# Optimization experiments

Hardware: AMD Instinct MI355X
Metric: run time of the kernel (lower is better)

The kernel has to match this reference:

```python
import jax, jax.numpy as jnp
import numpy as np

N = 8192          # num_nodes
F_IN = 512        # num_features
D = 256           # embedding_dim
C = 40            # num_classes
E = 262144        # num_edges (avg degree 32)
ALPHA = 0.5
LN_EPS = 1e-5


def _layer_norm(x, eps=LN_EPS):
    # F.layer_norm over last dim, no affine params
    mu = jnp.mean(x, axis=-1, keepdims=True)
    var = jnp.var(x, axis=-1, keepdims=True)
    return (x - mu) * jax.lax.rsqrt(var + eps)


def setup_inputs() -> dict:
    key = jax.random.key(0)
    ks = jax.random.split(key, 16)
    s_in = 1.0 / np.sqrt(F_IN)
    s_d = 1.0 / np.sqrt(D)
    inp = {
        "X": jax.random.normal(ks[0], (N, F_IN), dtype=jnp.float32),
        "edge_row": jnp.sort(jax.random.randint(ks[1], (E,), 0, N)),
        "edge_col": jax.random.randint(ks[2], (E,), 0, N),
        "edge_weight": jax.random.uniform(ks[3], (E,), dtype=jnp.float32),
        # MLP embedding: Linear(F_IN, D)
        "W_emb": jax.random.uniform(ks[4], (F_IN, D), minval=-s_in, maxval=s_in),
        "b_emb": jax.random.uniform(ks[5], (D,), minval=-s_in, maxval=s_in),
        # attention projections: Linear(D, D) x3
        "W_q": jax.random.uniform(ks[6], (D, D), minval=-s_d, maxval=s_d),
        "b_q": jax.random.uniform(ks[7], (D,), minval=-s_d, maxval=s_d),
        "W_k": jax.random.uniform(ks[8], (D, D), minval=-s_d, maxval=s_d),
        "b_k": jax.random.uniform(ks[9], (D,), minval=-s_d, maxval=s_d),
        "W_v": jax.random.uniform(ks[10], (D, D), minval=-s_d, maxval=s_d),
        "b_v": jax.random.uniform(ks[11], (D,), minval=-s_d, maxval=s_d),
        # GNN linear: Linear(D, D)
        "W_gnn": jax.random.uniform(ks[12], (D, D), minval=-s_d, maxval=s_d),
        "b_gnn": jax.random.uniform(ks[13], (D,), minval=-s_d, maxval=s_d),
        # classifier: Linear(D, C)
        "W_cls": jax.random.uniform(ks[14], (D, C), minval=-s_d, maxval=s_d),
        "b_cls": jax.random.uniform(ks[15], (C,), minval=-s_d, maxval=s_d),
    }
    return inp


def reference(X, edge_row, edge_col, edge_weight,
              W_emb, b_emb, W_q, b_q, W_k, b_k, W_v, b_v,
              W_gnn, b_gnn, W_cls, b_cls):
    # embedding MLP
    Z0 = X @ W_emb + b_emb                      # [N, D]
    # global attention with QK layer-norm
    Q = _layer_norm(Z0 @ W_q + b_q)             # [N, D]
    K = _layer_norm(Z0 @ W_k + b_k)             # [N, D]
    V = Z0 @ W_v + b_v                          # [N, D]
    scores = Q @ K.T                            # [N, N]
    attn = jax.nn.softmax(scores, axis=-1)      # [N, N]
    Z_A = attn @ V                              # [N, D]
    # sparse GNN branch: spmm(A, linear(Z0))
    H = Z0 @ W_gnn + b_gnn                      # [N, D]
    msg = H[edge_col] * edge_weight[:, None]    # [E, D]
    gnn_out = jax.ops.segment_sum(msg, edge_row, num_segments=N)  # [N, D]
    # weighted blend + classifier
    Z_out = (1.0 - ALPHA) * Z_A + ALPHA * gnn_out
    Y_hat = Z_out @ W_cls + b_cls               # [N, C]
    return (Y_hat, attn)
```

## Files before the change

### kernel.cpp

```cpp
#include <hip/hip_runtime.h>
#include <hip/hip_bf16.h>

#define N_NODES 8192
#define F_IN    512
#define DIM     256
#define NCLS    40

typedef __attribute__((ext_vector_type(8))) short bf16x8;
typedef __attribute__((ext_vector_type(4))) float f32x4;

#define MFMA16 __builtin_amdgcn_mfma_f32_16x16x32_bf16

static __device__ __forceinline__ unsigned short f2bf(float x) {
    __hip_bfloat16 h = __float2bfloat16(x);
    return *reinterpret_cast<unsigned short*>(&h);
}
static __device__ __forceinline__ float bf2f(unsigned short u) {
    union { unsigned int u32; float f; } v; v.u32 = ((unsigned int)u) << 16;
    return v.f;
}
static __device__ __forceinline__ void gll16(const void* g, void* l) {
    __builtin_amdgcn_global_load_lds(
        (const __attribute__((address_space(1))) unsigned int*)g,
        (__attribute__((address_space(3))) unsigned int*)l, 16, 0, 0);
}

__global__ __launch_bounds__(256) void split_kernel(
    const float* __restrict__ X,
    unsigned short* __restrict__ Xh, unsigned short* __restrict__ Xl)
{
    const size_t i = ((size_t)blockIdx.x * 256 + threadIdx.x) * 4;
    float4 v = *(const float4*)&X[i];
    ushort4 h, l;
    h.x = f2bf(v.x); l.x = f2bf(v.x - bf2f(h.x));
    h.y = f2bf(v.y); l.y = f2bf(v.y - bf2f(h.y));
    h.z = f2bf(v.z); l.z = f2bf(v.z - bf2f(h.z));
    h.w = f2bf(v.w); l.w = f2bf(v.w - bf2f(h.w));
    *(ushort4*)&Xh[i] = h;
    *(ushort4*)&Xl[i] = l;
}

__global__ __launch_bounds__(256) void wtrans_kernel(
    const float* __restrict__ W,
    unsigned short* __restrict__ WTh, unsigned short* __restrict__ WTl,
    int K, int N)
{
    __shared__ float tile[64][65];
    const int r0 = blockIdx.x * 64;
    const int c0 = blockIdx.y * 64;
    const int t = threadIdx.x;
    #pragma unroll
    for (int i = 0; i < 4; ++i) {
        int r = i * 16 + (t >> 4);
        int c = (t & 15) * 4;
        float4 v = *(const float4*)&W[(size_t)(r0 + r) * N + c0 + c];
        tile[r][c] = v.x; tile[r][c + 1] = v.y;
        tile[r][c + 2] = v.z; tile[r][c + 3] = v.w;
    }
    __syncthreads();
    #pragma unroll
    for (int i = 0; i < 4; ++i) {
        int c = i * 16 + (t >> 4);
        int r = (t & 15) * 4;
        ushort4 h, l;
        float x0 = tile[r][c],     x1 = tile[r + 1][c];
        float x2 = tile[r + 2][c], x3 = tile[r + 3][c];
        h.x = f2bf(x0); l.x = f2bf(x0 - bf2f(h.x));
        h.y = f2bf(x1); l.y = f2bf(x1 - bf2f(h.y));
        h.z = f2bf(x2); l.z = f2bf(x2 - bf2f(h.z));
        h.w = f2bf(x3); l.w = f2bf(x3 - bf2f(h.w));
        *(ushort4*)&WTh[(size_t)(c0 + c) * K + r0 + r] = h;
        *(ushort4*)&WTl[(size_t)(c0 + c) * K + r0 + r] = l;
    }
}

template<int KDIM, int OUTMODE>
__global__ __launch_bounds__(256) void mfma_gemm3_kernel(
    const unsigned short* __restrict__ Ah_, const unsigned short* __restrict__ Al_,
    const unsigned short* __restrict__ Bh_, const unsigned short* __restrict__ Bl_,
    const float* __restrict__ bias,
    void* __restrict__ C0, void* __restrict__ C1)
{
    __shared__ short Ah[64][32], Al[64][32], Bh[128][32], Bl[128][32];

    const int m0 = blockIdx.y * 64;
    const int n0 = blockIdx.x * 128;
    const int t = threadIdx.x, lane = t & 63, w = t >> 6;
    const int wm = w >> 1, wn = w & 1;
    const int fr = lane & 15, kb = lane >> 4;

    f32x4 acc[2][4] = {};

    for (int k0 = 0; k0 < KDIM; k0 += 32) {
        #pragma unroll
        for (int r = 0; r < 2; ++r) {
            int c = r * 256 + t;
            int tens = c >> 8, idx = c & 255;
            int row = idx >> 2, slot = idx & 3;
            const unsigned short* src =
                (tens ? Al_ : Ah_) + (size_t)(m0 + row) * KDIM + k0 + slot * 8;
            gll16(src, (char*)(tens ? &Al[0][0] : &Ah[0][0]) + idx * 16);
        }
        #pragma unroll
        for (int r = 0; r < 4; ++r) {
            int c = r * 256 + t;
            int tens = c >> 9, idx = c & 511;
            int row = idx >> 2, slot = idx & 3;
            const unsigned short* src =
                (tens ? Bl_ : Bh_) + (size_t)(n0 + row) * KDIM + k0 + slot * 8;
            gll16(src, (char*)(tens ? &Bl[0][0] : &Bh[0][0]) + idx * 16);
        }
        __syncthreads();

        bf16x8 ah[2], al[2], bh[4], bl[4];
        #pragma unroll
        for (int m = 0; m < 2; ++m) {
            int row = wm * 32 + m * 16 + fr;
            ah[m] = *(const bf16x8*)&Ah[row][kb * 8];
            al[m] = *(const bf16x8*)&Al[row][kb * 8];
        }
        #pragma unroll
        for (int n = 0; n < 4; ++n) {
            int col = wn * 64 + n * 16 + fr;
            bh[n] = *(const bf16x8*)&Bh[col][kb * 8];
            bl[n] = *(const bf16x8*)&Bl[col][kb * 8];
        }
        #pragma unroll
        for (int m = 0; m < 2; ++m)
            #pragma unroll
            for (int n = 0; n < 4; ++n) {
                acc[m][n] = MFMA16(ah[m], bh[n], acc[m][n], 0, 0, 0);
                acc[m][n] = MFMA16(ah[m], bl[n], acc[m][n], 0, 0, 0);
                acc[m][n] = MFMA16(al[m], bh[n], acc[m][n], 0, 0, 0);
            }
        __syncthreads();
    }

    #pragma unroll
    for (int m = 0; m < 2; ++m)
        #pragma unroll
        for (int e = 0; e < 4; ++e) {
            const int row = m0 + wm * 32 + m * 16 + kb * 4 + e;
            #pragma unroll
            for (int n = 0; n < 4; ++n) {
                const int col = n0 + wn * 64 + n * 16 + fr;
                float v = acc[m][n][e] + bias[col];
                if (OUTMODE == 0) {
                    ((float*)C0)[(size_t)row * 256 + col] = v;
                } else if (OUTMODE == 1) {
                    ((unsigned short*)C0)[(size_t)row * 256 + col] = f2bf(v);
                } else {
                    unsigned short h = f2bf(v);
                    ((unsigned short*)C0)[(size_t)row * 256 + col] = h;
                    ((unsigned short*)C1)[(size_t)row * 256 + col] =
                        f2bf(v - bf2f(h));
                }
            }
        }
}

__global__ __launch_bounds__(256) void ln_split_kernel(
    const float* __restrict__ X,
    unsigned short* __restrict__ Hi, unsigned short* __restrict__ Lo)
{
    const int row = blockIdx.x;
    const int t = threadIdx.x;
    float x = X[(size_t)row * DIM + t];

    float s1 = x, s2 = x * x;
    #pragma unroll
    for (int o = 32; o; o >>= 1) {
        s1 += __shfl_xor(s1, o);
        s2 += __shfl_xor(s2, o);
    }
    __shared__ float r1[4], r2[4];
    const int wid = t >> 6;
    if ((t & 63) == 0) { r1[wid] = s1; r2[wid] = s2; }
    __syncthreads();
    const float sum = r1[0] + r1[1] + r1[2] + r1[3];
    const float ssq = r2[0] + r2[1] + r2[2] + r2[3];
    const float mean = sum * (1.0f / DIM);
    const float var  = ssq * (1.0f / DIM) - mean * mean;
    const float y = (x - mean) * rsqrtf(var + 1e-5f);

    const unsigned short h = f2bf(y);
    Hi[(size_t)row * DIM + t] = h;
    Lo[(size_t)row * DIM + t] = f2bf(y - bf2f(h));
}

__global__ __launch_bounds__(256) void vtrans_kernel(
    const float* __restrict__ V, unsigned short* __restrict__ VT)
{
    __shared__ float tile[64][65];
    const int r0 = blockIdx.x * 64;
    const int c0 = blockIdx.y * 64;
    const int t = threadIdx.x;
    #pragma unroll
    for (int i = 0; i < 4; ++i) {
        int r = i * 16 + (t >> 4);
        int c = (t & 15) * 4;
        float4 v = *(const float4*)&V[(size_t)(r0 + r) * DIM + c0 + c];
        tile[r][c] = v.x; tile[r][c + 1] = v.y;
        tile[r][c + 2] = v.z; tile[r][c + 3] = v.w;
    }
    __syncthreads();
    #pragma unroll
    for (int i = 0; i < 4; ++i) {
        int c = i * 16 + (t >> 4);
        int r = (t & 15) * 4;
        ushort4 o;
        o.x = f2bf(tile[r][c]);     o.y = f2bf(tile[r + 1][c]);
        o.z = f2bf(tile[r + 2][c]); o.w = f2bf(tile[r + 3][c]);
        *(ushort4*)&VT[(size_t)(c0 + c) * N_NODES + r0 + r] = o;
    }
}

__global__ __launch_bounds__(256) void qkt_kernel(
    const unsigned short* __restrict__ Qh, const unsigned short* __restrict__ Ql,
    const unsigned short* __restrict__ Kh, const unsigned short* __restrict__ Kl,
    unsigned short* __restrict__ Sb, float2* __restrict__ pstat)
{
    __shared__ short stage[4][128][32];
    __shared__ float2 ps[2][128];
    __shared__ float gmr[128];

    const int bid = blockIdx.x;
    const int wg = (bid & 7) * 512 + (bid >> 3);
    const int mb = wg >> 6, nb = wg & 63;
    const int m0 = mb * 128, n0 = nb * 128;

    const int t = threadIdx.x, lane = t & 63, w = t >> 6;
    const int wm = w >> 1, wn = w & 1;
    const int fr = lane & 15, kb = lane >> 4;

    f32x4 acc[4][4] = {};

    for (int k0 = 0; k0 < DIM; k0 += 32) {
        #pragma unroll
        for (int r = 0; r < 2; ++r) {
            int c = r * 256 + t;
            int row = c >> 2, slot = c & 3;
            size_t ga = (size_t)(m0 + row) * DIM + k0 + slot * 8;
            size_t gb = (size_t)(n0 + row) * DIM + k0 + slot * 8;
            int lo = c * 16;
            gll16(Qh + ga, (char*)&stage[0][0][0] + lo);
            gll16(Ql + ga, (char*)&stage[1][0][0] + lo);
            gll16(Kh + gb, (char*)&stage[2][0][0] + lo);
            gll16(Kl + gb, (char*)&stage[3][0][0] + lo);
        }
        __syncthreads();

        bf16x8 ah[4], al[4], bh[4], bl[4];
        #pragma unroll
        for (int m = 0; m < 4; ++m) {
            int row = wm * 64 + m * 16 + fr;
            ah[m] = *(const bf16x8*)&stage[0][row][kb * 8];
            al[m] = *(const bf16x8*)&stage[1][row][kb * 8];
        }
        #pragma unroll
        for (int n = 0; n < 4; ++n) {
            int col = wn * 64 + n * 16 + fr;
            bh[n] = *(const bf16x8*)&stage[2][col][kb * 8];
            bl[n] = *(const bf16x8*)&stage[3][col][kb * 8];
        }
        #pragma unroll
        for (int m = 0; m < 4; ++m)
            #pragma unroll
            for (int n = 0; n < 4; ++n) {
                acc[m][n] = MFMA16(ah[m], bh[n], acc[m][n], 0, 0, 0);
                acc[m][n] = MFMA16(ah[m], bl[n], acc[m][n], 0, 0, 0);
                acc[m][n] = MFMA16(al[m], bh[n], acc[m][n], 0, 0, 0);
            }
        __syncthreads();
    }

    #pragma unroll
    for (int m = 0; m < 4; ++m)
        #pragma unroll
        for (int e = 0; e < 4; ++e) {
            float mx = acc[m][0][e];
            #pragma unroll
            for (int n = 1; n < 4; ++n) mx = fmaxf(mx, acc[m][n][e]);
            #pragma unroll
            for (int o = 1; o < 16; o <<= 1) mx = fmaxf(mx, __shfl_xor(mx, o));
            if (fr == 0) ps[wn][wm * 64 + m * 16 + kb * 4 + e].x = mx;
        }
    __syncthreads();
    if (t < 128) gmr[t] = fmaxf(ps[0][t].x, ps[1][t].x);
    __syncthreads();

    unsigned short* tile = (unsigned short*)&stage[0][0][0];
    #pragma unroll
    for (int m = 0; m < 4; ++m)
        #pragma unroll
        for (int e = 0; e < 4; ++e) {
            const int rl = wm * 64 + m * 16 + kb * 4 + e;
            const float g = gmr[rl];
            float se = 0.f;
            #pragma unroll
            for (int n = 0; n < 4; ++n) {
                float ev = __expf(acc[m][n][e] - g);
                se += ev;
                tile[rl * 128 + wn * 64 + n * 16 + fr] = f2bf(ev);
            }
            #pragma unroll
            for (int o = 1; o < 16; o <<= 1) se += __shfl_xor(se, o);
            if (fr == 0) ps[wn][rl].y = se;
        }
    __syncthreads();
    if (t < 128)
        pstat[(size_t)(m0 + t) * 64 + nb] =
            make_float2(gmr[t], ps[0][t].y + ps[1][t].y);

    #pragma unroll
    for (int p = 0; p < 8; ++p) {
        int c = p * 256 + t;
        int r = c >> 4, sl = c & 15;
        *(int4*)&Sb[(size_t)(m0 + r) * 16384 + n0 + sl * 8] =
            *(const int4*)((const char*)tile + c * 16);
    }
}

__global__ __launch_bounds__(256) void factor_kernel(
    const float2* __restrict__ pstat, float* __restrict__ factab)
{
    const int row = blockIdx.x * 4 + (threadIdx.x >> 6);
    const int lane = threadIdx.x & 63;
    float2 v = pstat[(size_t)row * 64 + lane];
    float gm = v.x;
    #pragma unroll
    for (int o = 1; o < 64; o <<= 1) gm = fmaxf(gm, __shfl_xor(gm, o));
    float s = v.y * __expf(v.x - gm);
    #pragma unroll
    for (int o = 1; o < 64; o <<= 1) s += __shfl_xor(s, o);
    factab[(size_t)row * 64 + lane] = __expf(v.x - gm) / s;
}

__global__ __launch_bounds__(256, 2) void av_mfma_kernel(
    const unsigned short* __restrict__ Sb, const float* __restrict__ factab,
    const unsigned short* __restrict__ VT,
    float* __restrict__ P0, float* __restrict__ P1,
    float* __restrict__ P2, float* __restrict__ P3)
{
    __shared__ unsigned short As[2][64][128];
    __shared__ float facsT[16][64];

    const int bid = blockIdx.x;
    const int rb = bid >> 2, ks = bid & 3;
    const int r0 = rb * 64, kbase = ks * 2048, cb0 = ks * 16;
    const int t = threadIdx.x, lane = t & 63, w = t >> 6;
    const int fr = lane & 15, kb = lane >> 4;

    for (int i = t; i < 1024; i += 256)
        facsT[i >> 6][i & 63] =
            factab[(size_t)(r0 + (i & 63)) * 64 + cb0 + (i >> 6)];

    const unsigned short* vb[4];
    #pragma unroll
    for (int n = 0; n < 4; ++n)
        vb[n] = VT + (size_t)(w * 64 + n * 16 + fr) * N_NODES + kbase + kb * 8;

    #define STAGE(S_, BUF_) do {                                              \
        _Pragma("unroll")                                                     \
        for (int p = 0; p < 4; ++p) {                                         \
            int c = p * 256 + t;                                              \
            int rr = c >> 4, sl = c & 15;                                     \
            int slp = sl ^ (rr & 7);                                          \
            gll16(Sb + (size_t)(r0 + rr) * 16384 + kbase + (S_) * 128 + slp * 8, \
                  (char*)&As[BUF_][0][0] + c * 16);                           \
        } } while (0)

    f32x4 acc[4][4] = {};
    const f32x4 z4 = {0.f, 0.f, 0.f, 0.f};

    STAGE(0, 0);
    __syncthreads();

    for (int s = 0; s < 16; ++s) {
        const int b = s & 1;
        if (s + 1 < 16) STAGE(s + 1, b ^ 1);

        bf16x8 bb[4][4];
        #pragma unroll
        for (int ksl = 0; ksl < 4; ++ksl)
            #pragma unroll
            for (int n = 0; n < 4; ++n)
                bb[ksl][n] = *(const bf16x8*)(vb[n] + s * 128 + ksl * 32);

        const char* abase = (const char*)&As[b][0][0];
        #pragma unroll
        for (int m = 0; m < 4; ++m) {
            f32x4 sacc[4];
            {
                bf16x8 a = *(const bf16x8*)(abase + (m * 16 + fr) * 256 +
                                            ((kb ^ (fr & 7)) * 16));
                #pragma unroll
                for (int n = 0; n < 4; ++n)
                    sacc[n] = MFMA16(a, bb[0][n], z4, 0, 0, 0);
            }
            #pragma unroll
            for (int ksl = 1; ksl < 4; ++ksl) {
                bf16x8 a = *(const bf16x8*)(abase + (m * 16 + fr) * 256 +
                                            (((ksl * 4 + kb) ^ (fr & 7)) * 16));
                #pragma unroll
                for (int n = 0; n < 4; ++n)
                    sacc[n] = MFMA16(a, bb[ksl][n], sacc[n], 0, 0, 0);
            }
            f32x4 fac = *(const f32x4*)&facsT[s][m * 16 + kb * 4];
            #pragma unroll
            for (int n = 0; n < 4; ++n)
                acc[m][n] += fac * sacc[n];
        }
        __syncthreads();
    }
    #undef STAGE

    float* P = (ks == 0) ? P0 : (ks == 1) ? P1 : (ks == 2) ? P2 : P3;
    #pragma unroll
    for (int m = 0; m < 4; ++m)
        #pragma unroll
        for (int e = 0; e < 4; ++e) {
            int row = r0 + m * 16 + kb * 4 + e;
            #pragma unroll
            for (int n = 0; n < 4; ++n)
                P[(size_t)row * DIM + w * 64 + n * 16 + fr] = acc[m][n][e];
        }
}

__global__ __launch_bounds__(256) void scale_kernel(
    const unsigned short* __restrict__ Sb, const float* __restrict__ factab,
    float* __restrict__ attn)
{
    const int row = blockIdx.x;
    const int t = threadIdx.x;
    const unsigned short* src = Sb + (size_t)row * 16384;

    int4 v[4];
    float f[4];
    #pragma unroll
    for (int p = 0; p < 4; ++p) {
        int c = p * 256 + t;
        v[p] = *(const int4*)&src[c * 8];
        f[p] = factab[(size_t)row * 64 + (c >> 4)];
    }
    __syncthreads();

    float* dst = attn + (size_t)row * N_NODES;
    #pragma unroll
    for (int p = 0; p < 4; ++p) {
        int c = p * 256 + t;
        float4 o0, o1;
        o0.x = bf2f((unsigned short)(v[p].x & 0xffff)) * f[p];
        o0.y = bf2f((unsigned short)((unsigned)v[p].x >> 16)) * f[p];
        o0.z = bf2f((unsigned short)(v[p].y & 0xffff)) * f[p];
        o0.w = bf2f((unsigned short)((unsigned)v[p].y >> 16)) * f[p];
        o1.x = bf2f((unsigned short)(v[p].z & 0xffff)) * f[p];
        o1.y = bf2f((unsigned short)((unsigned)v[p].z >> 16)) * f[p];
        o1.z = bf2f((unsigned short)(v[p].w & 0xffff)) * f[p];
        o1.w = bf2f((unsigned short)((unsigned)v[p].w >> 16)) * f[p];
        *(float4*)(dst + c * 8)     = o0;
        *(float4*)(dst + c * 8 + 4) = o1;
    }
}

__global__ __launch_bounds__(256) void spmm_kernel(
    const unsigned short* __restrict__ Hb, const int* __restrict__ erow,
    const int* __restrict__ ecol, const float* __restrict__ ew,
    float* __restrict__ out, int E)
{
    const int node = blockIdx.x * 4 + (threadIdx.x >> 6);
    const int lane = threadIdx.x & 63;

    int lo = 0, hi = E;
    while (lo < hi) { int mid = (lo + hi) >> 1; if (erow[mid] < node) lo = mid + 1; else hi = mid; }
    const int beg = lo;
    hi = E;
    while (lo < hi) { int mid = (lo + hi) >> 1; if (erow[mid] < node + 1) lo = mid + 1; else hi = mid; }
    const int end = lo;

    float4 acc = make_float4(0.f, 0.f, 0.f, 0.f);
    for (int e = beg; e < end; ++e) {
        const int col = ecol[e];
        const float wgt = ew[e];
        ushort4 h = *(const ushort4*)&Hb[(size_t)col * DIM + lane * 4];
        acc.x += wgt * bf2f(h.x);
        acc.y += wgt * bf2f(h.y);
        acc.z += wgt * bf2f(h.z);
        acc.w += wgt * bf2f(h.w);
    }
    *(float4*)&out[(size_t)node * DIM + lane * 4] = acc;
}

__global__ __launch_bounds__(256) void blend_cls_kernel(
    const float* __restrict__ p0, const float* __restrict__ p1,
    const float* __restrict__ p2, const float* __restrict__ p3,
    const float* __restrict__ gnn,
    const float* __restrict__ Wc, const float* __restrict__ bc,
    float* __restrict__ Y)
{
    const int row = blockIdx.x;
    const int t = threadIdx.x;
    __shared__ float z[DIM];
    __shared__ float part[4][NCLS];

    const size_t i = (size_t)row * DIM + t;
    z[t] = 0.5f * (p0[i] + p1[i] + p2[i] + p3[i] + gnn[i]);
    __syncthreads();

    if (t < 160) {
        const int c = t % NCLS, q = t / NCLS;
        float acc = 0.0f;
        #pragma unroll 4
        for (int d = q * 64; d < q * 64 + 64; ++d)
            acc += z[d] * Wc[d * NCLS + c];
        part[q][c] = acc;
    }
    __syncthreads();
    if (t < NCLS)
        Y[(size_t)row * NCLS + t] =
            part[0][t] + part[1][t] + part[2][t] + part[3][t] + bc[t];
}

extern "C" void kernel_launch(void* const* d_in, const int* in_sizes, int n_in,
                              void* d_out, int out_size, void* d_ws, size_t ws_size,
                              hipStream_t stream)
{
    const float* X     = (const float*)d_in[0];
    const int*   erow  = (const int*)d_in[1];
    const int*   ecol  = (const int*)d_in[2];
    const float* ew    = (const float*)d_in[3];
    const float* W_emb = (const float*)d_in[4];
    const float* b_emb = (const float*)d_in[5];
    const float* W_q   = (const float*)d_in[6];
    const float* b_q   = (const float*)d_in[7];
    const float* W_k   = (const float*)d_in[8];
    const float* b_k   = (const float*)d_in[9];
    const float* W_v   = (const float*)d_in[10];
    const float* b_v   = (const float*)d_in[11];
    const float* W_g   = (const float*)d_in[12];
    const float* b_g   = (const float*)d_in[13];
    const float* W_c   = (const float*)d_in[14];
    const float* b_c   = (const float*)d_in[15];
    const int E = in_sizes[1];

    float* Y    = (float*)d_out;
    float* Sc   = Y + (size_t)N_NODES * NCLS;
    unsigned short* Sb = (unsigned short*)Sc;

    const size_t ND = (size_t)N_NODES * DIM;
    float* R0 = (float*)d_ws;
    float* R1 = R0 + ND;
    float* R2 = R1 + ND;
    float* R3 = R2 + ND;
    float* R4 = R3 + ND;
    float* R5 = R4 + ND;
    float* R6 = R5 + ND;

    unsigned short* Xh = (unsigned short*)R0;
    unsigned short* Xl = (unsigned short*)R1;
    unsigned short* Wt = (unsigned short*)R2;
    unsigned short* WembTh = Wt;
    unsigned short* WembTl = Wt + 256 * 512;
    unsigned short* WqTh = WembTl + 256 * 512;
    unsigned short* WqTl = WqTh + 256 * 256;
    unsigned short* WkTh = WqTl + 256 * 256;
    unsigned short* WkTl = WkTh + 256 * 256;
    unsigned short* WvTh = WkTl + 256 * 256;
    unsigned short* WvTl = WvTh + 256 * 256;
    unsigned short* WgTh = WvTl + 256 * 256;
    unsigned short* WgTl = WgTh + 256 * 256;
    unsigned short* Z0h = (unsigned short*)R3;
    unsigned short* Z0l = Z0h + ND;
    float* Qf = R4;
    float* Kf = R5;
    float* Vf = R6;
    unsigned short* Hb = (unsigned short*)R0;
    unsigned short* Qh = (unsigned short*)R1;
    unsigned short* Ql = Qh + ND;
    unsigned short* Kh = (unsigned short*)R2;
    unsigned short* Kl = Kh + ND;
    unsigned short* VT = (unsigned short*)(R0 + ND / 2);
    float2* pstat = (float2*)R4;
    float*  factab = R5;
    float* P0 = R6;
    float* P1 = R3;
    float* P2 = R4;
    float* P3 = R1;
    float* GNN = R2;

    split_kernel<<<(N_NODES * F_IN) / 1024, 256, 0, stream>>>(X, Xh, Xl);

    wtrans_kernel<<<dim3(F_IN / 64, DIM / 64), 256, 0, stream>>>(W_emb, WembTh, WembTl, F_IN, DIM);
    wtrans_kernel<<<dim3(DIM / 64, DIM / 64), 256, 0, stream>>>(W_q, WqTh, WqTl, DIM, DIM);
    wtrans_kernel<<<dim3(DIM / 64, DIM / 64), 256, 0, stream>>>(W_k, WkTh, WkTl, DIM, DIM);
    wtrans_kernel<<<dim3(DIM / 64, DIM / 64), 256, 0, stream>>>(W_v, WvTh, WvTl, DIM, DIM);
    wtrans_kernel<<<dim3(DIM / 64, DIM / 64), 256, 0, stream>>>(W_g, WgTh, WgTl, DIM, DIM);

    mfma_gemm3_kernel<F_IN, 2><<<dim3(2, N_NODES / 64), 256, 0, stream>>>(
        Xh, Xl, WembTh, WembTl, b_emb, Z0h, Z0l);

    mfma_gemm3_kernel<DIM, 0><<<dim3(2, N_NODES / 64), 256, 0, stream>>>(
        Z0h, Z0l, WqTh, WqTl, b_q, Qf, nullptr);
    mfma_gemm3_kernel<DIM, 0><<<dim3(2, N_NODES / 64), 256, 0, stream>>>(
        Z0h, Z0l, WkTh, WkTl, b_k, Kf, nullptr);
    mfma_gemm3_kernel<DIM, 0><<<dim3(2, N_NODES / 64), 256, 0, stream>>>(
        Z0h, Z0l, WvTh, WvTl, b_v, Vf, nullptr);
    mfma_gemm3_kernel<DIM, 1><<<dim3(2, N_NODES / 64), 256, 0, stream>>>(
        Z0h, Z0l, WgTh, WgTl, b_g, Hb, nullptr);

    ln_split_kernel<<<N_NODES, 256, 0, stream>>>(Qf, Qh, Ql);
    ln_split_kernel<<<N_NODES, 256, 0, stream>>>(Kf, Kh, Kl);

    vtrans_kernel<<<dim3(N_NODES / 64, DIM / 64), 256, 0, stream>>>(Vf, VT);

    qkt_kernel<<<4096, 256, 0, stream>>>(Qh, Ql, Kh, Kl, Sb, pstat);

    factor_kernel<<<N_NODES / 4, 256, 0, stream>>>(pstat, factab);

    av_mfma_kernel<<<512, 256, 0, stream>>>(Sb, factab, VT, P0, P1, P2, P3);

    scale_kernel<<<N_NODES, 256, 0, stream>>>(Sb, factab, Sc);

    spmm_kernel<<<N_NODES / 4, 256, 0, stream>>>(Hb, erow, ecol, ew, GNN, E);

    blend_cls_kernel<<<N_NODES, 256, 0, stream>>>(
        P0, P1, P2, P3, GNN, W_c, b_c, Y);
}
```

Before: 476.4 us.

## Batch projection GEMMs, enlarge tiles, swizzle LDS and remap block order

The GEMM M-tile grows from 64 to 128 rows with launch bounds set to 2 blocks per SM. The four Z0 projections (Q, K, V, GNN) now run as one launch indexed by blockIdx.z instead of four separate kernels. Global-to-LDS load addresses are precomputed once and advanced by pointer increments. The QK^T kernel gets a new block-to-tile mapping for L2 locality, an XOR swizzle on its LDS exp tile to cut bank conflicts, and launch bounds of 4. The AV kernel block ordering is remapped in the same spirit. Larger tiles and these launch bounds may raise register pressure or reduce parallelism.

```diff
diff --git a/kernel.cpp b/kernel.cpp
--- a/kernel.cpp
+++ b/kernel.cpp
@@ -75,47 +75,46 @@
 }
 
 template<int KDIM, int OUTMODE>
-__global__ __launch_bounds__(256) void mfma_gemm3_kernel(
+__device__ __forceinline__ void gemm3_body(
     const unsigned short* __restrict__ Ah_, const unsigned short* __restrict__ Al_,
     const unsigned short* __restrict__ Bh_, const unsigned short* __restrict__ Bl_,
     const float* __restrict__ bias,
-    void* __restrict__ C0, void* __restrict__ C1)
-{
-    __shared__ short Ah[64][32], Al[64][32], Bh[128][32], Bl[128][32];
-
-    const int m0 = blockIdx.y * 64;
-    const int n0 = blockIdx.x * 128;
+    void* __restrict__ C0, void* __restrict__ C1,
+    int m0, int n0,
+    short (*Ah)[32], short (*Al)[32], short (*Bh)[32], short (*Bl)[32])
+{
     const int t = threadIdx.x, lane = t & 63, w = t >> 6;
     const int wm = w >> 1, wn = w & 1;
     const int fr = lane & 15, kb = lane >> 4;
 
-    f32x4 acc[2][4] = {};
+    const unsigned short* asrc[4];
+    const unsigned short* bsrc[4];
+    char* adst[4];
+    char* bdst[4];
+    #pragma unroll
+    for (int r = 0; r < 4; ++r) {
+        int c = r * 256 + t;
+        int tens = c >> 9, idx = c & 511;
+        int row = idx >> 2, slot = idx & 3;
+        asrc[r] = (tens ? Al_ : Ah_) + (size_t)(m0 + row) * KDIM + slot * 8;
+        adst[r] = (char*)(tens ? &Al[0][0] : &Ah[0][0]) + idx * 16;
+        bsrc[r] = (tens ? Bl_ : Bh_) + (size_t)(n0 + row) * KDIM + slot * 8;
+        bdst[r] = (char*)(tens ? &Bl[0][0] : &Bh[0][0]) + idx * 16;
+    }
+
+    f32x4 acc[4][4] = {};
 
     for (int k0 = 0; k0 < KDIM; k0 += 32) {
         #pragma unroll
-        for (int r = 0; r < 2; ++r) {
-            int c = r * 256 + t;
-            int tens = c >> 8, idx = c & 255;
-            int row = idx >> 2, slot = idx & 3;
-            const unsigned short* src =
-                (tens ? Al_ : Ah_) + (size_t)(m0 + row) * KDIM + k0 + slot * 8;
-            gll16(src, (char*)(tens ? &Al[0][0] : &Ah[0][0]) + idx * 16);
-        }
-        #pragma unroll
-        for (int r = 0; r < 4; ++r) {
-            int c = r * 256 + t;
-            int tens = c >> 9, idx = c & 511;
-            int row = idx >> 2, slot = idx & 3;
-            const unsigned short* src =
-                (tens ? Bl_ : Bh_) + (size_t)(n0 + row) * KDIM + k0 + slot * 8;
-            gll16(src, (char*)(tens ? &Bl[0][0] : &Bh[0][0]) + idx * 16);
-        }
+        for (int r = 0; r < 4; ++r) { gll16(asrc[r], adst[r]); asrc[r] += 32; }
+        #pragma unroll
+        for (int r = 0; r < 4; ++r) { gll16(bsrc[r], bdst[r]); bsrc[r] += 32; }
         __syncthreads();
 
-        bf16x8 ah[2], al[2], bh[4], bl[4];
-        #pragma unroll
-        for (int m = 0; m < 2; ++m) {
-            int row = wm * 32 + m * 16 + fr;
+        bf16x8 ah[4], al[4], bh[4], bl[4];
+        #pragma unroll
+        for (int m = 0; m < 4; ++m) {
+            int row = wm * 64 + m * 16 + fr;
             ah[m] = *(const bf16x8*)&Ah[row][kb * 8];
             al[m] = *(const bf16x8*)&Al[row][kb * 8];
         }
@@ -126,7 +125,7 @@
             bl[n] = *(const bf16x8*)&Bl[col][kb * 8];
         }
         #pragma unroll
-        for (int m = 0; m < 2; ++m)
+        for (int m = 0; m < 4; ++m)
             #pragma unroll
             for (int n = 0; n < 4; ++n) {
                 acc[m][n] = MFMA16(ah[m], bh[n], acc[m][n], 0, 0, 0);
@@ -137,10 +136,10 @@
     }
 
     #pragma unroll
-    for (int m = 0; m < 2; ++m)
+    for (int m = 0; m < 4; ++m)
         #pragma unroll
         for (int e = 0; e < 4; ++e) {
-            const int row = m0 + wm * 32 + m * 16 + kb * 4 + e;
+            const int row = m0 + wm * 64 + m * 16 + kb * 4 + e;
             #pragma unroll
             for (int n = 0; n < 4; ++n) {
                 const int col = n0 + wn * 64 + n * 16 + fr;
@@ -159,6 +158,42 @@
         }
 }
 
+template<int KDIM, int OUTMODE>
+__global__ __launch_bounds__(256, 2) void mfma_gemm3_kernel(
+    const unsigned short* __restrict__ Ah_, const unsigned short* __restrict__ Al_,
+    const unsigned short* __restrict__ Bh_, const unsigned short* __restrict__ Bl_,
+    const float* __restrict__ bias,
+    void* __restrict__ C0, void* __restrict__ C1)
+{
+    __shared__ short Ah[128][32], Al[128][32], Bh[128][32], Bl[128][32];
+    gemm3_body<KDIM, OUTMODE>(Ah_, Al_, Bh_, Bl_, bias, C0, C1,
+                              blockIdx.y * 128, blockIdx.x * 128,
+                              Ah, Al, Bh, Bl);
+}
+
+struct Proj4Args {
+    const unsigned short* Bh[4];
+    const unsigned short* Bl[4];
+    const float* bias[4];
+    void* C[4];
+};
+
+__global__ __launch_bounds__(256, 2) void proj4_kernel(
+    const unsigned short* __restrict__ Ah_, const unsigned short* __restrict__ Al_,
+    Proj4Args p)
+{
+    __shared__ short Ah[128][32], Al[128][32], Bh[128][32], Bl[128][32];
+    const int z = blockIdx.z;
+    if (z < 3)
+        gemm3_body<DIM, 0>(Ah_, Al_, p.Bh[z], p.Bl[z], p.bias[z], p.C[z],
+                           nullptr, blockIdx.y * 128, blockIdx.x * 128,
+                           Ah, Al, Bh, Bl);
+    else
+        gemm3_body<DIM, 1>(Ah_, Al_, p.Bh[z], p.Bl[z], p.bias[z], p.C[z],
+                           nullptr, blockIdx.y * 128, blockIdx.x * 128,
+                           Ah, Al, Bh, Bl);
+}
+
 __global__ __launch_bounds__(256) void ln_split_kernel(
     const float* __restrict__ X,
     unsigned short* __restrict__ Hi, unsigned short* __restrict__ Lo)
@@ -215,7 +250,7 @@
     }
 }
 
-__global__ __launch_bounds__(256) void qkt_kernel(
+__global__ __launch_bounds__(256, 4) void qkt_kernel(
     const unsigned short* __restrict__ Qh, const unsigned short* __restrict__ Ql,
     const unsigned short* __restrict__ Kh, const unsigned short* __restrict__ Kl,
     unsigned short* __restrict__ Sb, float2* __restrict__ pstat)
@@ -225,28 +260,45 @@
     __shared__ float gmr[128];
 
     const int bid = blockIdx.x;
-    const int wg = (bid & 7) * 512 + (bid >> 3);
-    const int mb = wg >> 6, nb = wg & 63;
+    const int x   = bid & 7;
+    const int i   = bid >> 3;
+    const int nbs = i >> 6;
+    const int j   = i & 63;
+    const int mb  = x * 8 + (j & 7);
+    const int nb  = nbs * 8 + (j >> 3);
     const int m0 = mb * 128, n0 = nb * 128;
 
     const int t = threadIdx.x, lane = t & 63, w = t >> 6;
     const int wm = w >> 1, wn = w & 1;
     const int fr = lane & 15, kb = lane >> 4;
 
+    const unsigned short* qsrc[2][2];
+    const unsigned short* ksrc[2][2];
+    char* qdst[2][2];
+    char* kdst[2][2];
+    #pragma unroll
+    for (int r = 0; r < 2; ++r) {
+        int c = r * 256 + t;
+        int row = c >> 2, slot = c & 3;
+        size_t ga = (size_t)(m0 + row) * DIM + slot * 8;
+        size_t gb = (size_t)(n0 + row) * DIM + slot * 8;
+        qsrc[r][0] = Qh + ga; qsrc[r][1] = Ql + ga;
+        ksrc[r][0] = Kh + gb; ksrc[r][1] = Kl + gb;
+        qdst[r][0] = (char*)&stage[0][0][0] + c * 16;
+        qdst[r][1] = (char*)&stage[1][0][0] + c * 16;
+        kdst[r][0] = (char*)&stage[2][0][0] + c * 16;
+        kdst[r][1] = (char*)&stage[3][0][0] + c * 16;
+    }
+
     f32x4 acc[4][4] = {};
 
     for (int k0 = 0; k0 < DIM; k0 += 32) {
         #pragma unroll
         for (int r = 0; r < 2; ++r) {
-            int c = r * 256 + t;
-            int row = c >> 2, slot = c & 3;
-            size_t ga = (size_t)(m0 + row) * DIM + k0 + slot * 8;
-            size_t gb = (size_t)(n0 + row) * DIM + k0 + slot * 8;
-            int lo = c * 16;
-            gll16(Qh + ga, (char*)&stage[0][0][0] + lo);
-            gll16(Ql + ga, (char*)&stage[1][0][0] + lo);
-            gll16(Kh + gb, (char*)&stage[2][0][0] + lo);
-            gll16(Kl + gb, (char*)&stage[3][0][0] + lo);
+            gll16(qsrc[r][0], qdst[r][0]); qsrc[r][0] += 32;
+            gll16(qsrc[r][1], qdst[r][1]); qsrc[r][1] += 32;
+            gll16(ksrc[r][0], kdst[r][0]); ksrc[r][0] += 32;
+            gll16(ksrc[r][1], kdst[r][1]); ksrc[r][1] += 32;
         }
         __syncthreads();
 
@@ -296,12 +348,15 @@
         for (int e = 0; e < 4; ++e) {
             const int rl = wm * 64 + m * 16 + kb * 4 + e;
             const float g = gmr[rl];
+            const int key = kb << 1;
             float se = 0.f;
             #pragma unroll
             for (int n = 0; n < 4; ++n) {
                 float ev = __expf(acc[m][n][e] - g);
                 se += ev;
-                tile[rl * 128 + wn * 64 + n * 16 + fr] = f2bf(ev);
+                const int col = wn * 64 + n * 16 + fr;
+                tile[rl * 128 + (((col >> 3) ^ key) << 3) + (col & 7)] =
+                    f2bf(ev);
             }
             #pragma unroll
             for (int o = 1; o < 16; o <<= 1) se += __shfl_xor(se, o);
@@ -316,8 +371,9 @@
     for (int p = 0; p < 8; ++p) {
         int c = p * 256 + t;
         int r = c >> 4, sl = c & 15;
+        int slx = sl ^ (((r >> 2) & 3) << 1);
         *(int4*)&Sb[(size_t)(m0 + r) * 16384 + n0 + sl * 8] =
-            *(const int4*)((const char*)tile + c * 16);
+            *(const int4*)((const char*)tile + (r * 16 + slx) * 16);
     }
 }
 
@@ -346,39 +402,49 @@
     __shared__ float facsT[16][64];
 
     const int bid = blockIdx.x;
-    const int rb = bid >> 2, ks = bid & 3;
+    const int x = bid & 7, i = bid >> 3;
+    const int ks = i >> 4;
+    const int rb = (i & 15) * 8 + x;
     const int r0 = rb * 64, kbase = ks * 2048, cb0 = ks * 16;
     const int t = threadIdx.x, lane = t & 63, w = t >> 6;
     const int fr = lane & 15, kb = lane >> 4;
 
-    for (int i = t; i < 1024; i += 256)
-        facsT[i >> 6][i & 63] =
-            factab[(size_t)(r0 + (i & 63)) * 64 + cb0 + (i >> 6)];
+    for (int ii = t; ii < 1024; ii += 256)
+        facsT[ii >> 6][ii & 63] =
+            factab[(size_t)(r0 + (ii & 63)) * 64 + cb0 + (ii >> 6)];
 
     const unsigned short* vb[4];
     #pragma unroll
     for (int n = 0; n < 4; ++n)
         vb[n] = VT + (size_t)(w * 64 + n * 16 + fr) * N_NODES + kbase + kb * 8;
 
-    #define STAGE(S_, BUF_) do {                                              \
+    const unsigned short* ssrc[4];
+    char* sdst[4];
+    #pragma unroll
+    for (int p = 0; p < 4; ++p) {
+        int c = p * 256 + t;
+        int rr = c >> 4, sl = c & 15;
+        int slp = sl ^ (rr & 7);
+        ssrc[p] = Sb + (size_t)(r0 + rr) * 16384 + kbase + slp * 8;
+        sdst[p] = (char*)&As[0][0][0] + c * 16;
+    }
+
+    #define STAGE(BUF_) do {                                                  \
         _Pragma("unroll")                                                     \
         for (int p = 0; p < 4; ++p) {                                         \
-            int c = p * 256 + t;                                              \
-            int rr = c >> 4, sl = c & 15;                                     \
-            int slp = sl ^ (rr & 7);                                          \
-            gll16(Sb + (size_t)(r0 + rr) * 16384 + kbase + (S_) * 128 + slp * 8, \
-                  (char*)&As[BUF_][0][0] + c * 16);                           \
+            gll16(ssrc[p], sdst[p] + (BUF_) * 16384);                         \
+            ssrc[p] += 128;                                                   \
         } } while (0)
 
     f32x4 acc[4][4] = {};
     const f32x4 z4 = {0.f, 0.f, 0.f, 0.f};
 
-    STAGE(0, 0);
+    STAGE(0);
     __syncthreads();
 
     for (int s = 0; s < 16; ++s) {
         const int b = s & 1;
-        if (s + 1 < 16) STAGE(s + 1, b ^ 1);
+        if (s + 1 < 16) STAGE(b ^ 1);
 
         bf16x8 bb[4][4];
         #pragma unroll
@@ -596,17 +662,15 @@
     wtrans_kernel<<<dim3(DIM / 64, DIM / 64), 256, 0, stream>>>(W_v, WvTh, WvTl, DIM, DIM);
     wtrans_kernel<<<dim3(DIM / 64, DIM / 64), 256, 0, stream>>>(W_g, WgTh, WgTl, DIM, DIM);
 
-    mfma_gemm3_kernel<F_IN, 2><<<dim3(2, N_NODES / 64), 256, 0, stream>>>(
+    mfma_gemm3_kernel<F_IN, 2><<<dim3(2, N_NODES / 128), 256, 0, stream>>>(
         Xh, Xl, WembTh, WembTl, b_emb, Z0h, Z0l);
 
-    mfma_gemm3_kernel<DIM, 0><<<dim3(2, N_NODES / 64), 256, 0, stream>>>(
-        Z0h, Z0l, WqTh, WqTl, b_q, Qf, nullptr);
-    mfma_gemm3_kernel<DIM, 0><<<dim3(2, N_NODES / 64), 256, 0, stream>>>(
-        Z0h, Z0l, WkTh, WkTl, b_k, Kf, nullptr);
-    mfma_gemm3_kernel<DIM, 0><<<dim3(2, N_NODES / 64), 256, 0, stream>>>(
-        Z0h, Z0l, WvTh, WvTl, b_v, Vf, nullptr);
-    mfma_gemm3_kernel<DIM, 1><<<dim3(2, N_NODES / 64), 256, 0, stream>>>(
-        Z0h, Z0l, WgTh, WgTl, b_g, Hb, nullptr);
+    Proj4Args pa;
+    pa.Bh[0] = WqTh; pa.Bl[0] = WqTl; pa.bias[0] = b_q; pa.C[0] = Qf;
+    pa.Bh[1] = WkTh; pa.Bl[1] = WkTl; pa.bias[1] = b_k; pa.C[1] = Kf;
+    pa.Bh[2] = WvTh; pa.Bl[2] = WvTl; pa.bias[2] = b_v; pa.C[2] = Vf;
+    pa.Bh[3] = WgTh; pa.Bl[3] = WgTl; pa.bias[3] = b_g; pa.C[3] = Hb;
+    proj4_kernel<<<dim3(2, N_NODES / 128, 4), 256, 0, stream>>>(Z0h, Z0l, pa);
 
     ln_split_kernel<<<N_NODES, 256, 0, stream>>>(Qf, Qh, Ql);
     ln_split_kernel<<<N_NODES, 256, 0, stream>>>(Kf, Kh, Kl);
```

Result: faster. 429.8 us (-9.8%).
